# Performance work log

Measured on AMD Instinct MI355X. Metric: run time of the kernel, lower is better.

The kernel has to match this reference:

```python
import jax, jax.numpy as jnp
import numpy as np

ATTRACTION_W = 1.0
REPULSION_W = 1.0
MARGIN = 0.3  # hardcoded local `margin = 0.3` in the torch forward


def setup_inputs() -> dict:
    key = jax.random.key(0)
    k1, k2, k3 = jax.random.split(key, 3)
    B, N, D, K = 16, 65536, 32, 512
    beta = jax.random.normal(k1, (B, N, 1), dtype=jnp.float32)
    embed = jax.random.normal(k2, (B, N, D), dtype=jnp.float32)
    # instance id per hit: -1 = background, 0..K-1 = instances
    sid = jax.random.randint(k3, (B, N), -1, K).astype(jnp.int32)
    # first K hits are the condensation points, one per instance
    sid = sid.at[:, :K].set(jnp.arange(K, dtype=jnp.int32)[None, :])
    is_cp = jnp.zeros((B, N), dtype=jnp.int32).at[:, :K].set(1)
    return {"beta": beta, "embed": embed, "slice_id": sid, "is_cp": is_cp, "num_instances": K}


def _per_batch(beta_b, emb_b, sid, iscp, K):
    # beta_b: [N], emb_b: [N, D], sid/iscp: [N]
    N = sid.shape[0]
    cp = iscp == 1
    valid = sid >= 0
    noncp = valid & ~cp  # non-cp signal hits
    pos = cp.sum().astype(jnp.float32)
    neg = jnp.float32(N) - pos  # noncp + background
    pos_w = jax.lax.stop_gradient(neg / (pos + 1e-6))
    w = jnp.where(cp, pos_w, jnp.where(noncp, 1.0, 2.0))
    # weighted BCE-with-logits, reduction='mean'
    x = beta_b
    y = cp.astype(jnp.float32)
    bce = jnp.maximum(x, 0.0) - x * y + jnp.log1p(jnp.exp(-jnp.abs(x)))
    beta_ce = (w * bce).mean()

    # segment id: valid hits -> sid, background -> dummy segment K (dropped)
    seg = jnp.where(valid, sid, K)
    counts = jax.ops.segment_sum(valid.astype(jnp.float32), seg, num_segments=K + 1)[:K]
    inst_exists = counts > 0  # the `unique()` set

    # first cp hit index per instance (sentinel N if instance has no cp)
    idxs = jnp.arange(N)
    first_cp = jax.ops.segment_min(jnp.where(cp & valid, idxs, N), seg, num_segments=K + 1)[:K]
    has_cp = first_cp < N
    safe_cp = jnp.minimum(first_cp, N - 1)
    cp_emb = emb_b[safe_cp]  # [K, D]
    cp_beta = beta_b[safe_cp]  # [K]

    # attraction: sum over instances (with a cp) of mean ||e_hit - e_cp||^2
    sid_c = jnp.clip(sid, 0, K - 1)
    d2 = ((emb_b - cp_emb[sid_c]) ** 2).sum(-1)  # [N]
    d2 = jnp.where(valid, d2, 0.0)
    seg_d2 = jax.ops.segment_sum(d2, seg, num_segments=K + 1)[:K]
    attr = (jnp.where(has_cp & inst_exists, seg_d2 / jnp.maximum(counts, 1.0), 0.0).sum()
            * ATTRACTION_W)

    # ranking: instances with exactly 1 cp and >0 noncp hits
    cp_count = jax.ops.segment_sum((cp & valid).astype(jnp.float32), seg, num_segments=K + 1)[:K]
    ncp_count = jax.ops.segment_sum(noncp.astype(jnp.float32), seg, num_segments=K + 1)[:K]
    r = jax.nn.relu(beta_b + MARGIN - cp_beta[sid_c])
    r = jnp.where(noncp, r, 0.0)
    seg_r = jax.ops.segment_sum(r, seg, num_segments=K + 1)[:K]
    qual = (cp_count == 1.0) & (ncp_count > 0)
    n_unique = inst_exists.sum().astype(jnp.float32)
    ranking = (jnp.where(qual, seg_r / jnp.maximum(ncp_count, 1.0), 0.0).sum()
               / jnp.maximum(n_unique, 1.0))

    beta_loss = beta_ce + 2.0 * ranking

    # repulsion over all cp hits; data has exactly one cp per instance so the
    # cp set equals cp_emb (K points), matching torch's emb_b[cp_idx]
    diff = cp_emb[:, None, :] - cp_emb[None, :, :]  # [K, K, D]
    rep = jnp.exp(-(diff ** 2).sum(-1)).mean() * REPULSION_W

    return beta_loss + attr + rep, beta_loss, attr, rep


def reference(beta, embed, slice_id, is_cp, num_instances):
    K = int(num_instances)
    beta2 = beta[..., 0]  # squeeze(-1)
    loss_b, bl, al, rl = jax.vmap(lambda b, e, s, c: _per_batch(b, e, s, c, K))(
        beta2, embed, slice_id, is_cp)
    return loss_b.mean(), bl.mean(), al.mean(), rl.mean()
```

## Files before the change

### kernel.cpp

```cpp
#include <hip/hip_runtime.h>
#include <math.h>

#define N_HITS 65536
#define K_INST 512
#define MARGIN 0.3f
#define MAXB   16
#define BPB    32
#define HITS_PB (N_HITS / BPB)

__device__ int    g_cnt[MAXB * K_INST];
__device__ float  g_d2v[MAXB * K_INST];
__device__ float  g_rv [MAXB * K_INST];
__device__ int    g_fcp[MAXB * K_INST];
__device__ float  g_cpbeta[MAXB * K_INST];
__device__ float4 g_cpemb[MAXB * K_INST * 8];
__device__ int    g_pcc[MAXB * BPB * K_INST];
__device__ float  g_pcd[MAXB * BPB * K_INST];
__device__ float  g_pcr[MAXB * BPB * K_INST];
__device__ int    g_pos[MAXB];
__device__ float  g_scp[MAXB], g_sncp[MAXB], g_sbg[MAXB];
__device__ float  g_attr[MAXB], g_rank[MAXB], g_nuq[MAXB], g_rep[MAXB];
__device__ int    g_ctr;

__global__ __launch_bounds__(256) void k_init() {
    int i = blockIdx.x * 256 + threadIdx.x;
    if (i < MAXB * K_INST) {
        g_cnt[i] = 0; g_d2v[i] = 0.f; g_rv[i] = 0.f;
        g_fcp[i] = 0x7F7F7F7F;
    }
    if (i < MAXB) {
        g_pos[i] = 0; g_scp[i] = 0.f; g_sncp[i] = 0.f; g_sbg[i] = 0.f;
        g_attr[i] = 0.f; g_rank[i] = 0.f; g_nuq[i] = 0.f; g_rep[i] = 0.f;
    }
    if (i == 0) g_ctr = 0;
}

__global__ __launch_bounds__(256) void k_scan(
    const int* __restrict__ sid, const int* __restrict__ iscp) {
    int b = blockIdx.y;
    size_t bo = (size_t)b * N_HITS;
    int i = blockIdx.x * 256 + threadIdx.x;
    int stride = gridDim.x * 256;
    for (; i < N_HITS; i += stride) {
        int c = iscp[bo + i];
        if (c == 1) {
            atomicAdd(&g_pos[b], 1);
            int s = sid[bo + i];
            if (s >= 0) atomicMin(&g_fcp[b * K_INST + s], i);
        }
    }
}

__global__ __launch_bounds__(256) void k_gather(
    const float* __restrict__ beta, const float4* __restrict__ embed4, int B) {
    int g = blockIdx.x * 256 + threadIdx.x;
    int total = B * K_INST * 8;
    if (g >= total) return;
    int row = g >> 3, sub = g & 7;
    int b = row / K_INST;
    int fc = g_fcp[row];
    int safe = min(fc, N_HITS - 1);
    float4 e = embed4[((size_t)b * N_HITS + safe) * 8 + sub];
    g_cpemb[(size_t)row * 8 + sub] = e;
    if (sub == 0) g_cpbeta[row] = beta[b * N_HITS + safe];
}

__global__ __launch_bounds__(256) void k_bce(
    const float* __restrict__ beta,
    const int* __restrict__ sid_g, const int* __restrict__ iscp_g, int B) {
    __shared__ float l_cb[K_INST];
    __shared__ int   l_cnt[K_INST];
    __shared__ float l_r[K_INST];
    __shared__ float l_red[12];

    int b = blockIdx.y, tid = threadIdx.x;
    size_t bo = (size_t)b * N_HITS;
    int base = blockIdx.x * HITS_PB;

    for (int k = tid; k < K_INST; k += 256) {
        l_cnt[k] = 0; l_r[k] = 0.f;
        l_cb[k] = g_cpbeta[b * K_INST + k];
    }
    __syncthreads();

    float a_cp = 0.f, a_ncp = 0.f, a_bg = 0.f;
    int sv[8], cv[8];
    float xv[8];
#pragma unroll
    for (int i = 0; i < 8; ++i) {
        size_t h = bo + base + i * 256 + tid;
        sv[i] = sid_g[h];
        cv[i] = iscp_g[h];
        xv[i] = beta[h];
    }
#pragma unroll
    for (int i = 0; i < 8; ++i) {
        int s = sv[i];
        bool cp = (cv[i] == 1), valid = (s >= 0), noncp = valid && !cp;
        float x = xv[i];
        float t = __expf(-fabsf(x));
        float bce = fmaxf(x, 0.f) - (cp ? x : 0.f) + __logf(1.f + t);
        if (cp) a_cp += bce; else if (noncp) a_ncp += bce; else a_bg += bce;
        if (valid) {
            atomicAdd(&l_cnt[s], cp ? (1 << 20) : 1);
            if (noncp) {
                float r = x + MARGIN - l_cb[s];
                if (r > 0.f) atomicAdd(&l_r[s], r);
            }
        }
    }

    for (int o = 32; o > 0; o >>= 1) {
        a_cp  += __shfl_down(a_cp, o);
        a_ncp += __shfl_down(a_ncp, o);
        a_bg  += __shfl_down(a_bg, o);
    }
    int wave = tid >> 6;
    if ((tid & 63) == 0) { l_red[wave] = a_cp; l_red[4 + wave] = a_ncp; l_red[8 + wave] = a_bg; }
    __syncthreads();
    if (tid == 0) {
        atomicAdd(&g_scp[b],  l_red[0] + l_red[1] + l_red[2]  + l_red[3]);
        atomicAdd(&g_sncp[b], l_red[4] + l_red[5] + l_red[6]  + l_red[7]);
        atomicAdd(&g_sbg[b],  l_red[8] + l_red[9] + l_red[10] + l_red[11]);
    }
    size_t po = ((size_t)b * BPB + blockIdx.x) * K_INST;
    for (int k = tid; k < K_INST; k += 256) {
        g_pcc[po + k] = l_cnt[k];
        g_pcr[po + k] = l_r[k];
    }
}

__global__ __launch_bounds__(512, 4) void k_d2(
    const float4* __restrict__ embed4,
    const int* __restrict__ sid_g, int B) {
    __shared__ float4 l_cp[K_INST * 8];
    __shared__ float  l_d2[K_INST];

    int b = blockIdx.y, tid = threadIdx.x;
    size_t bo = (size_t)b * N_HITS;
    int base = blockIdx.x * HITS_PB;

    {
        const float4* cpt = g_cpemb + (size_t)b * K_INST * 8;
        for (int idx = tid; idx < K_INST * 8; idx += 512) {
            int k = idx >> 3, j = idx & 7;
            l_cp[(k << 3) | (j ^ (k & 7))] = cpt[idx];
        }
    }
    for (int k = tid; k < K_INST; k += 512) l_d2[k] = 0.f;
    __syncthreads();

    int sub = tid & 7, hgrp = tid >> 3;
#pragma unroll
    for (int g = 0; g < 4; ++g) {
        float4 e[8];
        int sv[8];
#pragma unroll
        for (int k = 0; k < 8; ++k) {
            int hit = base + (g * 8 + k) * 64 + hgrp;
            sv[k] = sid_g[bo + hit];
            e[k]  = embed4[(bo + hit) * 8 + sub];
        }
#pragma unroll
        for (int k = 0; k < 8; ++k) {
            int s = sv[k];
            int row = max(s, 0);
            float4 c4 = l_cp[(row << 3) | (sub ^ (row & 7))];
            float dx = e[k].x - c4.x, dy = e[k].y - c4.y;
            float dz = e[k].z - c4.z, dw = e[k].w - c4.w;
            float q = dx * dx + dy * dy + dz * dz + dw * dw;
            q += __shfl_xor(q, 1);
            q += __shfl_xor(q, 2);
            q += __shfl_xor(q, 4);
            if (sub == 0 && s >= 0) atomicAdd(&l_d2[s], q);
        }
    }

    __syncthreads();
    size_t po = ((size_t)b * BPB + blockIdx.x) * K_INST;
    for (int k = tid; k < K_INST; k += 512) g_pcd[po + k] = l_d2[k];
}

__global__ __launch_bounds__(256) void k_reduce() {
    __shared__ int   rc[4][64];
    __shared__ float rd[4][64];
    __shared__ float rr[4][64];
    int kl = threadIdx.x & 63, p4 = threadIdx.x >> 6;
    int bin = blockIdx.x * 64 + kl;
    int b = bin / K_INST;
    size_t basep = ((size_t)b * BPB) * K_INST + (bin % K_INST);
    int cs = 0; float ds = 0.f, rs = 0.f;
    for (int p = p4 * (BPB / 4); p < (p4 + 1) * (BPB / 4); ++p) {
        cs += g_pcc[basep + (size_t)p * K_INST];
        ds += g_pcd[basep + (size_t)p * K_INST];
        rs += g_pcr[basep + (size_t)p * K_INST];
    }
    rc[p4][kl] = cs; rd[p4][kl] = ds; rr[p4][kl] = rs;
    __syncthreads();
    if (p4 == 0) {
        g_cnt[bin] = rc[0][kl] + rc[1][kl] + rc[2][kl] + rc[3][kl];
        g_d2v[bin] = rd[0][kl] + rd[1][kl] + rd[2][kl] + rd[3][kl];
        g_rv[bin]  = rr[0][kl] + rr[1][kl] + rr[2][kl] + rr[3][kl];
    }
}

__global__ __launch_bounds__(512) void k_tail(float* out, int B) {
    int tid = threadIdx.x;
    int nrep = B * 16;

    if ((int)blockIdx.x < nrep) {
        __shared__ float4 tile[32 * 8];
        __shared__ float red[8];
        int b = blockIdx.x >> 4, t2 = blockIdx.x & 15;
        const float4* base = g_cpemb + (size_t)b * K_INST * 8;
        float4 r0[8];
#pragma unroll
        for (int cc = 0; cc < 8; ++cc) r0[cc] = base[(size_t)tid * 8 + cc];
        if (tid < 256) tile[tid] = base[(size_t)t2 * 256 + tid];
        __syncthreads();
        float acc = 0.f;
        for (int j = 0; j < 32; ++j) {
            float d2 = 0.f;
#pragma unroll
            for (int cc = 0; cc < 8; ++cc) {
                float4 ev = tile[j * 8 + cc];
                float ax = r0[cc].x - ev.x, ay = r0[cc].y - ev.y;
                float az = r0[cc].z - ev.z, aw = r0[cc].w - ev.w;
                d2 += ax * ax + ay * ay + az * az + aw * aw;
            }
            acc += __expf(-d2);
        }
        for (int o = 32; o > 0; o >>= 1) acc += __shfl_down(acc, o);
        if ((tid & 63) == 0) red[tid >> 6] = acc;
        __syncthreads();
        if (tid == 0) {
            float t = 0.f;
            for (int w = 0; w < 8; ++w) t += red[w];
            atomicAdd(&g_rep[b], t);
        }
    } else {
        __shared__ float red2[3][8];
        int b = blockIdx.x - nrep, k = tid;
        int v = g_cnt[b * K_INST + k];
        int ncp = v & 0xFFFFF, cpc = v >> 20;
        int counts = ncp + cpc;
        int fc = g_fcp[b * K_INST + k];
        bool has_cp = fc < N_HITS, exists = counts > 0;
        float segd = g_d2v[b * K_INST + k];
        float attr = (has_cp && exists) ? segd / fmaxf((float)counts, 1.f) : 0.f;
        float rank = (cpc == 1 && ncp > 0) ? g_rv[b * K_INST + k] / fmaxf((float)ncp, 1.f) : 0.f;
        float uq = exists ? 1.f : 0.f;
        for (int o = 32; o > 0; o >>= 1) {
            attr += __shfl_down(attr, o);
            rank += __shfl_down(rank, o);
            uq   += __shfl_down(uq, o);
        }
        if ((k & 63) == 0) { red2[0][k >> 6] = attr; red2[1][k >> 6] = rank; red2[2][k >> 6] = uq; }
        __syncthreads();
        if (k == 0) {
            float a = 0.f, r = 0.f, u = 0.f;
            for (int w = 0; w < 8; ++w) { a += red2[0][w]; r += red2[1][w]; u += red2[2][w]; }
            g_attr[b] = a; g_rank[b] = r; g_nuq[b] = u;
        }
    }

    __shared__ int is_last;
    __syncthreads();
    if (tid == 0) {
        __threadfence();
        int v = atomicAdd(&g_ctr, 1);
        is_last = (v == (int)gridDim.x - 1);
    }
    __syncthreads();
    if (is_last) {
        __threadfence();
        if (tid < 64) {
            int b = tid;
            float loss = 0.f, bl = 0.f, at = 0.f, rp = 0.f;
            if (b < B) {
                float pos = (float)g_pos[b];
                float pw = ((float)N_HITS - pos) / (pos + 1e-6f);
                float bce = (pw * g_scp[b] + g_sncp[b] + 2.f * g_sbg[b]) / (float)N_HITS;
                float rank = g_rank[b] / fmaxf(g_nuq[b], 1.f);
                bl = bce + 2.f * rank;
                at = g_attr[b];
                rp = g_rep[b] / (float)(K_INST * K_INST);
                loss = bl + at + rp;
            }
            for (int o = 32; o > 0; o >>= 1) {
                loss += __shfl_down(loss, o);
                bl   += __shfl_down(bl, o);
                at   += __shfl_down(at, o);
                rp   += __shfl_down(rp, o);
            }
            if (tid == 0) {
                float inv = 1.f / (float)B;
                out[0] = loss * inv;
                out[1] = bl * inv;
                out[2] = at * inv;
                out[3] = rp * inv;
            }
        }
    }
}

extern "C" void kernel_launch(void* const* d_in, const int* in_sizes, int n_in,
                              void* d_out, int out_size, void* d_ws, size_t ws_size,
                              hipStream_t stream) {
    const float*  beta   = (const float*)d_in[0];
    const float*  embed  = (const float*)d_in[1];
    const int*    sid    = (const int*)d_in[2];
    const int*    iscp   = (const int*)d_in[3];
    float* out = (float*)d_out;

    int BN = in_sizes[0];
    int B  = BN / N_HITS;
    if (B > MAXB) B = MAXB;
    int BK = B * K_INST;

    (void)d_ws; (void)ws_size;

    k_init<<<(MAXB * K_INST + 255) / 256, 256, 0, stream>>>();

    k_scan<<<dim3(32, B), 256, 0, stream>>>(sid, iscp);

    k_gather<<<(BK * 8 + 255) / 256, 256, 0, stream>>>(beta, (const float4*)embed, B);

    k_bce<<<dim3(BPB, B), 256, 0, stream>>>(beta, sid, iscp, B);

    k_d2<<<dim3(BPB, B), 512, 0, stream>>>((const float4*)embed, sid, B);

    k_reduce<<<BK / 64, 256, 0, stream>>>();

    k_tail<<<B * 16 + B, 512, 0, stream>>>(out, B);
}
```

Before: 251.7 us.

## Fuse all loss stages into one persistent kernel with grid barriers

Replaces the seven kernel launches with a single persistent kernel of 256 blocks that uses spin-wait global barriers between the init, cp-scan, gather, main accumulation and tail phases. The BCE and attraction distance passes now share one read of each hit, with each thread loading a full 32-float embedding row. Per-block partial arrays and the separate reduce kernel are replaced by global atomics. Repulsion reuses the shared-memory cp tile. This removes launch overhead and intermediate global traffic. In exchange it depends on all 256 blocks being co-resident for the barriers to avoid deadlock, and it adds global atomic contention.

Result: slower. 295.3 us (+17.3%).

```diff
diff --git a/kernel.cpp b/kernel.cpp
--- a/kernel.cpp
+++ b/kernel.cpp
@@ -1,12 +1,13 @@
 #include <hip/hip_runtime.h>
 #include <math.h>
 
-#define N_HITS 65536
-#define K_INST 512
-#define MARGIN 0.3f
-#define MAXB   16
-#define BPB    32
-#define HITS_PB (N_HITS / BPB)
+#define N_HITS  65536
+#define K_INST  512
+#define MARGIN  0.3f
+#define MAXB    16
+#define NBLK    256
+#define TPB     512
+#define HITS_PB 4096
 
 __device__ int    g_cnt[MAXB * K_INST];
 __device__ float  g_d2v[MAXB * K_INST];
@@ -14,216 +15,185 @@
 __device__ int    g_fcp[MAXB * K_INST];
 __device__ float  g_cpbeta[MAXB * K_INST];
 __device__ float4 g_cpemb[MAXB * K_INST * 8];
-__device__ int    g_pcc[MAXB * BPB * K_INST];
-__device__ float  g_pcd[MAXB * BPB * K_INST];
-__device__ float  g_pcr[MAXB * BPB * K_INST];
 __device__ int    g_pos[MAXB];
 __device__ float  g_scp[MAXB], g_sncp[MAXB], g_sbg[MAXB];
 __device__ float  g_attr[MAXB], g_rank[MAXB], g_nuq[MAXB], g_rep[MAXB];
 __device__ int    g_ctr;
-
-__global__ __launch_bounds__(256) void k_init() {
-    int i = blockIdx.x * 256 + threadIdx.x;
-    if (i < MAXB * K_INST) {
-        g_cnt[i] = 0; g_d2v[i] = 0.f; g_rv[i] = 0.f;
-        g_fcp[i] = 0x7F7F7F7F;
-    }
-    if (i < MAXB) {
-        g_pos[i] = 0; g_scp[i] = 0.f; g_sncp[i] = 0.f; g_sbg[i] = 0.f;
-        g_attr[i] = 0.f; g_rank[i] = 0.f; g_nuq[i] = 0.f; g_rep[i] = 0.f;
-    }
-    if (i == 0) g_ctr = 0;
+__device__ int    g_bar[4];
+
+__device__ __forceinline__ void gbar(int id) {
+    __syncthreads();
+    if (threadIdx.x == 0) {
+        __threadfence();
+        atomicAdd(&g_bar[id], 1);
+        while (__hip_atomic_load(&g_bar[id], __ATOMIC_RELAXED,
+                                 __HIP_MEMORY_SCOPE_AGENT) < NBLK)
+            __builtin_amdgcn_s_sleep(16);
+        __threadfence();
+    }
+    __syncthreads();
 }
 
-__global__ __launch_bounds__(256) void k_scan(
-    const int* __restrict__ sid, const int* __restrict__ iscp) {
-    int b = blockIdx.y;
+__global__ __launch_bounds__(TPB, 4) void k_all(
+    const float*  __restrict__ beta,
+    const float4* __restrict__ embed4,
+    const int*    __restrict__ sid_g,
+    const int*    __restrict__ iscp_g,
+    float* out, int B) {
+    __shared__ float4 l_cp[K_INST * 8];
+    __shared__ float  l_cb[K_INST];
+    __shared__ int    l_cnt[K_INST];
+    __shared__ float  l_r[K_INST];
+    __shared__ float  l_d2[K_INST];
+    __shared__ float  l_red[24];
+    __shared__ int    is_last;
+
+    int bi = blockIdx.x, tid = threadIdx.x;
+    int b  = bi >> 4;
+    int q  = bi & 15;
     size_t bo = (size_t)b * N_HITS;
-    int i = blockIdx.x * 256 + threadIdx.x;
-    int stride = gridDim.x * 256;
-    for (; i < N_HITS; i += stride) {
-        int c = iscp[bo + i];
-        if (c == 1) {
-            atomicAdd(&g_pos[b], 1);
-            int s = sid[bo + i];
-            if (s >= 0) atomicMin(&g_fcp[b * K_INST + s], i);
-        }
-    }
-}
-
-__global__ __launch_bounds__(256) void k_gather(
-    const float* __restrict__ beta, const float4* __restrict__ embed4, int B) {
-    int g = blockIdx.x * 256 + threadIdx.x;
-    int total = B * K_INST * 8;
-    if (g >= total) return;
-    int row = g >> 3, sub = g & 7;
-    int b = row / K_INST;
-    int fc = g_fcp[row];
-    int safe = min(fc, N_HITS - 1);
-    float4 e = embed4[((size_t)b * N_HITS + safe) * 8 + sub];
-    g_cpemb[(size_t)row * 8 + sub] = e;
-    if (sub == 0) g_cpbeta[row] = beta[b * N_HITS + safe];
-}
-
-__global__ __launch_bounds__(256) void k_bce(
-    const float* __restrict__ beta,
-    const int* __restrict__ sid_g, const int* __restrict__ iscp_g, int B) {
-    __shared__ float l_cb[K_INST];
-    __shared__ int   l_cnt[K_INST];
-    __shared__ float l_r[K_INST];
-    __shared__ float l_red[12];
-
-    int b = blockIdx.y, tid = threadIdx.x;
-    size_t bo = (size_t)b * N_HITS;
-    int base = blockIdx.x * HITS_PB;
-
-    for (int k = tid; k < K_INST; k += 256) {
-        l_cnt[k] = 0; l_r[k] = 0.f;
-        l_cb[k] = g_cpbeta[b * K_INST + k];
-    }
-    __syncthreads();
-
-    float a_cp = 0.f, a_ncp = 0.f, a_bg = 0.f;
-    int sv[8], cv[8];
-    float xv[8];
-#pragma unroll
-    for (int i = 0; i < 8; ++i) {
-        size_t h = bo + base + i * 256 + tid;
-        sv[i] = sid_g[h];
-        cv[i] = iscp_g[h];
-        xv[i] = beta[h];
-    }
-#pragma unroll
-    for (int i = 0; i < 8; ++i) {
-        int s = sv[i];
-        bool cp = (cv[i] == 1), valid = (s >= 0), noncp = valid && !cp;
-        float x = xv[i];
-        float t = __expf(-fabsf(x));
-        float bce = fmaxf(x, 0.f) - (cp ? x : 0.f) + __logf(1.f + t);
-        if (cp) a_cp += bce; else if (noncp) a_ncp += bce; else a_bg += bce;
-        if (valid) {
-            atomicAdd(&l_cnt[s], cp ? (1 << 20) : 1);
-            if (noncp) {
-                float r = x + MARGIN - l_cb[s];
-                if (r > 0.f) atomicAdd(&l_r[s], r);
-            }
-        }
-    }
-
-    for (int o = 32; o > 0; o >>= 1) {
-        a_cp  += __shfl_down(a_cp, o);
-        a_ncp += __shfl_down(a_ncp, o);
-        a_bg  += __shfl_down(a_bg, o);
-    }
-    int wave = tid >> 6;
-    if ((tid & 63) == 0) { l_red[wave] = a_cp; l_red[4 + wave] = a_ncp; l_red[8 + wave] = a_bg; }
-    __syncthreads();
-    if (tid == 0) {
-        atomicAdd(&g_scp[b],  l_red[0] + l_red[1] + l_red[2]  + l_red[3]);
-        atomicAdd(&g_sncp[b], l_red[4] + l_red[5] + l_red[6]  + l_red[7]);
-        atomicAdd(&g_sbg[b],  l_red[8] + l_red[9] + l_red[10] + l_red[11]);
-    }
-    size_t po = ((size_t)b * BPB + blockIdx.x) * K_INST;
-    for (int k = tid; k < K_INST; k += 256) {
-        g_pcc[po + k] = l_cnt[k];
-        g_pcr[po + k] = l_r[k];
-    }
-}
-
-__global__ __launch_bounds__(512, 4) void k_d2(
-    const float4* __restrict__ embed4,
-    const int* __restrict__ sid_g, int B) {
-    __shared__ float4 l_cp[K_INST * 8];
-    __shared__ float  l_d2[K_INST];
-
-    int b = blockIdx.y, tid = threadIdx.x;
-    size_t bo = (size_t)b * N_HITS;
-    int base = blockIdx.x * HITS_PB;
+    int base = q * HITS_PB;
+    bool act = (b < B);
 
     {
+        int i = bi * TPB + tid;
+        if (i < MAXB * K_INST) {
+            g_cnt[i] = 0; g_d2v[i] = 0.f; g_rv[i] = 0.f; g_fcp[i] = N_HITS;
+        }
+        if (i < MAXB) {
+            g_pos[i] = 0; g_scp[i] = 0.f; g_sncp[i] = 0.f; g_sbg[i] = 0.f;
+            g_attr[i] = 0.f; g_rank[i] = 0.f; g_nuq[i] = 0.f; g_rep[i] = 0.f;
+        }
+    }
+    gbar(0);
+
+    if (act) {
+        int pc = 0;
+#pragma unroll
+        for (int i = 0; i < HITS_PB / TPB; ++i) {
+            int h = base + i * TPB + tid;
+            int c = iscp_g[bo + h];
+            if (c == 1) {
+                ++pc;
+                int s = sid_g[bo + h];
+                if (s >= 0) atomicMin(&g_fcp[b * K_INST + s], h);
+            }
+        }
+        for (int o = 32; o > 0; o >>= 1) pc += __shfl_down(pc, o);
+        if ((tid & 63) == 0 && pc) atomicAdd(&g_pos[b], pc);
+    }
+    gbar(1);
+
+    if (act && tid < 256) {
+        int k = q * 32 + (tid >> 3), sub = tid & 7;
+        int row = b * K_INST + k;
+        int fc = g_fcp[row];
+        int safe = min(fc, N_HITS - 1);
+        float4 e = embed4[(bo + safe) * 8 + sub];
+        g_cpemb[(size_t)row * 8 + sub] = e;
+        if (sub == 0) g_cpbeta[row] = beta[bo + safe];
+    }
+    gbar(2);
+
+    if (act) {
         const float4* cpt = g_cpemb + (size_t)b * K_INST * 8;
-        for (int idx = tid; idx < K_INST * 8; idx += 512) {
+#pragma unroll
+        for (int it = 0; it < (K_INST * 8) / TPB; ++it) {
+            int idx = it * TPB + tid;
             int k = idx >> 3, j = idx & 7;
             l_cp[(k << 3) | (j ^ (k & 7))] = cpt[idx];
         }
-    }
-    for (int k = tid; k < K_INST; k += 512) l_d2[k] = 0.f;
-    __syncthreads();
-
-    int sub = tid & 7, hgrp = tid >> 3;
-#pragma unroll
-    for (int g = 0; g < 4; ++g) {
-        float4 e[8];
-        int sv[8];
-#pragma unroll
-        for (int k = 0; k < 8; ++k) {
-            int hit = base + (g * 8 + k) * 64 + hgrp;
-            sv[k] = sid_g[bo + hit];
-            e[k]  = embed4[(bo + hit) * 8 + sub];
-        }
-#pragma unroll
-        for (int k = 0; k < 8; ++k) {
-            int s = sv[k];
-            int row = max(s, 0);
-            float4 c4 = l_cp[(row << 3) | (sub ^ (row & 7))];
-            float dx = e[k].x - c4.x, dy = e[k].y - c4.y;
-            float dz = e[k].z - c4.z, dw = e[k].w - c4.w;
-            float q = dx * dx + dy * dy + dz * dz + dw * dw;
-            q += __shfl_xor(q, 1);
-            q += __shfl_xor(q, 2);
-            q += __shfl_xor(q, 4);
-            if (sub == 0 && s >= 0) atomicAdd(&l_d2[s], q);
-        }
-    }
-
-    __syncthreads();
-    size_t po = ((size_t)b * BPB + blockIdx.x) * K_INST;
-    for (int k = tid; k < K_INST; k += 512) g_pcd[po + k] = l_d2[k];
-}
-
-__global__ __launch_bounds__(256) void k_reduce() {
-    __shared__ int   rc[4][64];
-    __shared__ float rd[4][64];
-    __shared__ float rr[4][64];
-    int kl = threadIdx.x & 63, p4 = threadIdx.x >> 6;
-    int bin = blockIdx.x * 64 + kl;
-    int b = bin / K_INST;
-    size_t basep = ((size_t)b * BPB) * K_INST + (bin % K_INST);
-    int cs = 0; float ds = 0.f, rs = 0.f;
-    for (int p = p4 * (BPB / 4); p < (p4 + 1) * (BPB / 4); ++p) {
-        cs += g_pcc[basep + (size_t)p * K_INST];
-        ds += g_pcd[basep + (size_t)p * K_INST];
-        rs += g_pcr[basep + (size_t)p * K_INST];
-    }
-    rc[p4][kl] = cs; rd[p4][kl] = ds; rr[p4][kl] = rs;
-    __syncthreads();
-    if (p4 == 0) {
-        g_cnt[bin] = rc[0][kl] + rc[1][kl] + rc[2][kl] + rc[3][kl];
-        g_d2v[bin] = rd[0][kl] + rd[1][kl] + rd[2][kl] + rd[3][kl];
-        g_rv[bin]  = rr[0][kl] + rr[1][kl] + rr[2][kl] + rr[3][kl];
-    }
-}
-
-__global__ __launch_bounds__(512) void k_tail(float* out, int B) {
-    int tid = threadIdx.x;
-    int nrep = B * 16;
-
-    if ((int)blockIdx.x < nrep) {
-        __shared__ float4 tile[32 * 8];
-        __shared__ float red[8];
-        int b = blockIdx.x >> 4, t2 = blockIdx.x & 15;
-        const float4* base = g_cpemb + (size_t)b * K_INST * 8;
+        l_cb[tid] = g_cpbeta[b * K_INST + tid];
+        l_cnt[tid] = 0; l_r[tid] = 0.f; l_d2[tid] = 0.f;
+    }
+    __syncthreads();
+
+    float a_cp = 0.f, a_ncp = 0.f, a_bg = 0.f;
+    if (act) {
+        int sv[8], cv[8];
+        float xv[8];
+#pragma unroll
+        for (int i = 0; i < 8; ++i) {
+            size_t h = bo + base + i * TPB + tid;
+            sv[i] = sid_g[h];
+            cv[i] = iscp_g[h];
+            xv[i] = beta[h];
+        }
+#pragma unroll
+        for (int pp = 0; pp < 4; ++pp) {
+            float4 e[2][8];
+#pragma unroll
+            for (int i = 0; i < 2; ++i) {
+                size_t ebase = (bo + base + (pp * 2 + i) * TPB + tid) * 8;
+#pragma unroll
+                for (int j = 0; j < 8; ++j) e[i][j] = embed4[ebase + j];
+            }
+#pragma unroll
+            for (int i = 0; i < 2; ++i) {
+                int hi = pp * 2 + i;
+                int s = sv[hi];
+                bool cp = (cv[hi] == 1), valid = (s >= 0), noncp = valid && !cp;
+                float x = xv[hi];
+                float t = __expf(-fabsf(x));
+                float bce = fmaxf(x, 0.f) - (cp ? x : 0.f) + __logf(1.f + t);
+                if (cp) a_cp += bce; else if (noncp) a_ncp += bce; else a_bg += bce;
+
+                int sc = max(s, 0);
+                int rowb = sc << 3, sw = sc & 7;
+                float d2 = 0.f;
+#pragma unroll
+                for (int j = 0; j < 8; ++j) {
+                    float4 cc = l_cp[rowb | (j ^ sw)];
+                    float dx = e[i][j].x - cc.x, dy = e[i][j].y - cc.y;
+                    float dz = e[i][j].z - cc.z, dw = e[i][j].w - cc.w;
+                    d2 += dx * dx + dy * dy + dz * dz + dw * dw;
+                }
+                if (valid) {
+                    atomicAdd(&l_cnt[s], cp ? (1 << 20) : 1);
+                    atomicAdd(&l_d2[s], d2);
+                    if (noncp) {
+                        float r = x + MARGIN - l_cb[s];
+                        if (r > 0.f) atomicAdd(&l_r[s], r);
+                    }
+                }
+            }
+        }
+
+        for (int o = 32; o > 0; o >>= 1) {
+            a_cp  += __shfl_down(a_cp, o);
+            a_ncp += __shfl_down(a_ncp, o);
+            a_bg  += __shfl_down(a_bg, o);
+        }
+        int wave = tid >> 6;
+        if ((tid & 63) == 0) { l_red[wave] = a_cp; l_red[8 + wave] = a_ncp; l_red[16 + wave] = a_bg; }
+    }
+    __syncthreads();
+    if (act) {
+        if (tid == 0) {
+            float t0 = 0.f, t1 = 0.f, t2 = 0.f;
+            for (int w = 0; w < 8; ++w) { t0 += l_red[w]; t1 += l_red[8 + w]; t2 += l_red[16 + w]; }
+            atomicAdd(&g_scp[b], t0);
+            atomicAdd(&g_sncp[b], t1);
+            atomicAdd(&g_sbg[b], t2);
+        }
+        int cc = l_cnt[tid]; if (cc) atomicAdd(&g_cnt[b * K_INST + tid], cc);
+        float dv = l_d2[tid]; if (dv != 0.f) atomicAdd(&g_d2v[b * K_INST + tid], dv);
+        float rv = l_r[tid];  if (rv != 0.f) atomicAdd(&g_rv[b * K_INST + tid], rv);
+    }
+    gbar(3);
+
+    if (act) {
+        int sw = tid & 7;
         float4 r0[8];
 #pragma unroll
-        for (int cc = 0; cc < 8; ++cc) r0[cc] = base[(size_t)tid * 8 + cc];
-        if (tid < 256) tile[tid] = base[(size_t)t2 * 256 + tid];
-        __syncthreads();
+        for (int cc = 0; cc < 8; ++cc) r0[cc] = l_cp[(tid << 3) | (cc ^ sw)];
         float acc = 0.f;
-        for (int j = 0; j < 32; ++j) {
+        for (int j = q * 32; j < q * 32 + 32; ++j) {
+            int jw = j & 7;
             float d2 = 0.f;
 #pragma unroll
             for (int cc = 0; cc < 8; ++cc) {
-                float4 ev = tile[j * 8 + cc];
+                float4 ev = l_cp[(j << 3) | (cc ^ jw)];
                 float ax = r0[cc].x - ev.x, ay = r0[cc].y - ev.y;
                 float az = r0[cc].z - ev.z, aw = r0[cc].w - ev.w;
                 d2 += ax * ax + ay * ay + az * az + aw * aw;
@@ -231,60 +201,62 @@
             acc += __expf(-d2);
         }
         for (int o = 32; o > 0; o >>= 1) acc += __shfl_down(acc, o);
-        if ((tid & 63) == 0) red[tid >> 6] = acc;
-        __syncthreads();
-        if (tid == 0) {
-            float t = 0.f;
-            for (int w = 0; w < 8; ++w) t += red[w];
-            atomicAdd(&g_rep[b], t);
-        }
-    } else {
-        __shared__ float red2[3][8];
-        int b = blockIdx.x - nrep, k = tid;
-        int v = g_cnt[b * K_INST + k];
-        int ncp = v & 0xFFFFF, cpc = v >> 20;
-        int counts = ncp + cpc;
-        int fc = g_fcp[b * K_INST + k];
-        bool has_cp = fc < N_HITS, exists = counts > 0;
-        float segd = g_d2v[b * K_INST + k];
-        float attr = (has_cp && exists) ? segd / fmaxf((float)counts, 1.f) : 0.f;
-        float rank = (cpc == 1 && ncp > 0) ? g_rv[b * K_INST + k] / fmaxf((float)ncp, 1.f) : 0.f;
-        float uq = exists ? 1.f : 0.f;
+        int wave = tid >> 6;
+        if ((tid & 63) == 0) l_red[wave] = acc;
+    }
+    __syncthreads();
+    if (act && tid == 0) {
+        float t = 0.f;
+        for (int w = 0; w < 8; ++w) t += l_red[w];
+        atomicAdd(&g_rep[b], t);
+    }
+
+    if (act && tid < 64) {
+        bool vld = tid < 32;
+        int bin = bi * 32 + (vld ? tid : 0);
+        float attr = 0.f, rank = 0.f, uq = 0.f;
+        if (vld) {
+            int v = g_cnt[bin];
+            int ncp = v & 0xFFFFF, cpc = v >> 20;
+            int counts = ncp + cpc;
+            int fc = g_fcp[bin];
+            bool has_cp = fc < N_HITS, exists = counts > 0;
+            attr = (has_cp && exists) ? g_d2v[bin] / fmaxf((float)counts, 1.f) : 0.f;
+            rank = (cpc == 1 && ncp > 0) ? g_rv[bin] / fmaxf((float)ncp, 1.f) : 0.f;
+            uq = exists ? 1.f : 0.f;
+        }
         for (int o = 32; o > 0; o >>= 1) {
             attr += __shfl_down(attr, o);
             rank += __shfl_down(rank, o);
             uq   += __shfl_down(uq, o);
         }
-        if ((k & 63) == 0) { red2[0][k >> 6] = attr; red2[1][k >> 6] = rank; red2[2][k >> 6] = uq; }
-        __syncthreads();
-        if (k == 0) {
-            float a = 0.f, r = 0.f, u = 0.f;
-            for (int w = 0; w < 8; ++w) { a += red2[0][w]; r += red2[1][w]; u += red2[2][w]; }
-            g_attr[b] = a; g_rank[b] = r; g_nuq[b] = u;
-        }
-    }
-
-    __shared__ int is_last;
+        if (tid == 0) {
+            if (attr != 0.f) atomicAdd(&g_attr[b], attr);
+            if (rank != 0.f) atomicAdd(&g_rank[b], rank);
+            if (uq != 0.f)   atomicAdd(&g_nuq[b], uq);
+        }
+    }
+
     __syncthreads();
     if (tid == 0) {
         __threadfence();
         int v = atomicAdd(&g_ctr, 1);
-        is_last = (v == (int)gridDim.x - 1);
+        is_last = (v == NBLK - 1);
     }
     __syncthreads();
     if (is_last) {
         __threadfence();
         if (tid < 64) {
-            int b = tid;
+            int bb = tid;
             float loss = 0.f, bl = 0.f, at = 0.f, rp = 0.f;
-            if (b < B) {
-                float pos = (float)g_pos[b];
+            if (bb < B) {
+                float pos = (float)g_pos[bb];
                 float pw = ((float)N_HITS - pos) / (pos + 1e-6f);
-                float bce = (pw * g_scp[b] + g_sncp[b] + 2.f * g_sbg[b]) / (float)N_HITS;
-                float rank = g_rank[b] / fmaxf(g_nuq[b], 1.f);
+                float bce = (pw * g_scp[bb] + g_sncp[bb] + 2.f * g_sbg[bb]) / (float)N_HITS;
+                float rank = g_rank[bb] / fmaxf(g_nuq[bb], 1.f);
                 bl = bce + 2.f * rank;
-                at = g_attr[b];
-                rp = g_rep[b] / (float)(K_INST * K_INST);
+                at = g_attr[bb];
+                rp = g_rep[bb] / (float)(K_INST * K_INST);
                 loss = bl + at + rp;
             }
             for (int o = 32; o > 0; o >>= 1) {
@@ -300,6 +272,10 @@
                 out[2] = at * inv;
                 out[3] = rp * inv;
             }
+        }
+        if (tid == 64) {
+            g_ctr = 0;
+            g_bar[0] = 0; g_bar[1] = 0; g_bar[2] = 0; g_bar[3] = 0;
         }
     }
 }
@@ -316,21 +292,9 @@
     int BN = in_sizes[0];
     int B  = BN / N_HITS;
     if (B > MAXB) B = MAXB;
-    int BK = B * K_INST;
 
     (void)d_ws; (void)ws_size;
 
-    k_init<<<(MAXB * K_INST + 255) / 256, 256, 0, stream>>>();
-
-    k_scan<<<dim3(32, B), 256, 0, stream>>>(sid, iscp);
-
-    k_gather<<<(BK * 8 + 255) / 256, 256, 0, stream>>>(beta, (const float4*)embed, B);
-
-    k_bce<<<dim3(BPB, B), 256, 0, stream>>>(beta, sid, iscp, B);
-
-    k_d2<<<dim3(BPB, B), 512, 0, stream>>>((const float4*)embed, sid, B);
-
-    k_reduce<<<BK / 64, 256, 0, stream>>>();
-
-    k_tail<<<B * 16 + B, 512, 0, stream>>>(out, B);
+    k_all<<<NBLK, TPB, 0, stream>>>(beta, (const float4*)embed, sid, iscp,
+                                    out, B);
 }
```
